# Optimization experiments

Measured on AMD Instinct MI355X. Metric: run time of the kernel, lower is better.

The kernel has to match this reference:

```python
import jax, jax.numpy as jnp
import numpy as np

THRESHOLD = 0.3
NEG_BIG = -2.0 ** 32  # matches tf -2**32 causal mask constant


def setup_inputs() -> dict:
    key = jax.random.key(0)
    kq, kt, kv = jax.random.split(key, 3)
    B, S, D = 16, 2048, 128
    Q = jax.random.normal(kq, (B, S, D), dtype=jnp.float32)
    T = jax.random.normal(kt, (B, S, D), dtype=jnp.float32)
    V = jax.random.normal(kv, (B, S, D), dtype=jnp.float32)
    return {"Q": Q, "T": T, "V": V}


def reference(Q, T, V):
    # scores: [B, S, S]
    A = jnp.einsum('bqd,bkd->bqk', Q, T)
    # Faithful to tf.where(A>thr, A, -2**32 * cast(A>thr)):
    # the false branch evaluates to 0 (mask is 0 there), NOT -2**32.
    A = jnp.where(A > THRESHOLD, A, jnp.zeros((), A.dtype))
    S = Q.shape[1]
    causal = jnp.triu(jnp.ones((S, S), dtype=bool), k=1)  # strictly upper = masked
    A = A + jnp.where(causal, jnp.asarray(NEG_BIG, A.dtype), jnp.zeros((), A.dtype))
    d_k = jnp.asarray(Q.shape[-1], A.dtype)
    A = A / jnp.sqrt(d_k)
    y = jax.nn.softmax(A, axis=-1)
    return jnp.einsum('bqk,bkd->bqd', y, V)
```

## Files before the change

### kernel.cpp

```cpp
#include <hip/hip_runtime.h>
#include <hip/hip_bf16.h>


#define S_LEN 2048
#define D_DIM 128
#define BQ 64
#define BK 64
#define THRESH 0.3f
#define SCALE 0.08838834764831845f

typedef __bf16 bf16x8 __attribute__((ext_vector_type(8)));
typedef float f32x4 __attribute__((ext_vector_type(4)));

__global__ void vt_kernel(const float* __restrict__ V, __bf16* __restrict__ Vt) {
    __shared__ float tile[64][65];
    int bid = blockIdx.x;
    int b  = bid >> 6;
    int t2 = bid & 63;
    int s0 = (t2 >> 1) * 64;
    int d0 = (t2 & 1) * 64;
    int tid = threadIdx.x;
    #pragma unroll
    for (int it = 0; it < 2; ++it) {
        int row = it * 32 + (tid >> 3);
        int c   = (tid & 7) * 8;
        const float* p = V + ((size_t)b * S_LEN + s0 + row) * D_DIM + d0 + c;
        *(f32x4*)(&tile[row][c])     = *(const f32x4*)p;
        *(f32x4*)(&tile[row][c + 4]) = *(const f32x4*)(p + 4);
    }
    __syncthreads();
    #pragma unroll
    for (int it = 0; it < 2; ++it) {
        int dr = it * 32 + (tid >> 3);
        int c  = (tid & 7) * 8;
        bf16x8 w;
        #pragma unroll
        for (int j = 0; j < 8; ++j) w[j] = (__bf16)tile[c + j][dr];
        *(bf16x8*)(Vt + ((size_t)b * D_DIM + d0 + dr) * S_LEN + s0 + c) = w;
    }
}

__global__ __launch_bounds__(256, 2)
void fa_kernel(const float* __restrict__ Q, const float* __restrict__ T,
               const __bf16* __restrict__ Vt, float* __restrict__ O) {
    __shared__ __bf16 Tt[64 * 136];
    __shared__ __bf16 Vl[128 * 72];
    __shared__ __bf16 Pl[4][16 * 72];

    int bid  = blockIdx.x;
    int b    = bid & 15;
    int half = bid >> 8;
    int idx  = (bid >> 4) & 15;
    int qt   = half == 0 ? (31 - idx) : idx;
    int q0   = qt * BQ;

    int tid  = threadIdx.x;
    int lane = tid & 63;
    int wave = tid >> 6;
    int col  = lane & 15;
    int quad = lane >> 4;

    const float* qptr = Q + ((size_t)b * S_LEN + (q0 + wave * 16 + col)) * D_DIM + quad * 8;
    bf16x8 qf[4];
    #pragma unroll
    for (int kk = 0; kk < 4; ++kk) {
        f32x4 a = *(const f32x4*)(qptr + kk * 32);
        f32x4 c = *(const f32x4*)(qptr + kk * 32 + 4);
        #pragma unroll
        for (int j = 0; j < 4; ++j) { qf[kk][j] = (__bf16)a[j]; qf[kk][4 + j] = (__bf16)c[j]; }
    }

    f32x4 oacc[8];
    #pragma unroll
    for (int dt = 0; dt < 8; ++dt) oacc[dt] = {0.f, 0.f, 0.f, 0.f};
    float lsum[4] = {0.f, 0.f, 0.f, 0.f};

    f32x4 tr[8]; bf16x8 vr[4];
    auto loadTiles = [&](int k0) {
        #pragma unroll
        for (int it = 0; it < 4; ++it) {
            int flat = it * 2048 + tid * 8;
            int row = flat >> 7, c = flat & 127;
            const float* p = T + ((size_t)b * S_LEN + k0 + row) * D_DIM + c;
            tr[2 * it]     = *(const f32x4*)p;
            tr[2 * it + 1] = *(const f32x4*)(p + 4);
        }
        #pragma unroll
        for (int it = 0; it < 4; ++it) {
            int flat = it * 2048 + tid * 8;
            int d = flat >> 6, kk2 = flat & 63;
            vr[it] = *(const bf16x8*)(Vt + ((size_t)b * D_DIM + d) * S_LEN + k0 + kk2);
        }
    };
    auto storeTiles = [&]() {
        #pragma unroll
        for (int it = 0; it < 4; ++it) {
            int flat = it * 2048 + tid * 8;
            int row = flat >> 7, c = flat & 127;
            bf16x8 w;
            #pragma unroll
            for (int j = 0; j < 4; ++j) {
                w[j]     = (__bf16)tr[2 * it][j];
                w[4 + j] = (__bf16)tr[2 * it + 1][j];
            }
            *(bf16x8*)(&Tt[row * 136 + c]) = w;
        }
        #pragma unroll
        for (int it = 0; it < 4; ++it) {
            int flat = it * 2048 + tid * 8;
            int d = flat >> 6, kk2 = flat & 63;
            *(bf16x8*)(&Vl[d * 72 + kk2]) = vr[it];
        }
    };

    loadTiles(0);
    storeTiles();
    __syncthreads();

    for (int kt = 0; kt <= qt; ++kt) {
        if (kt < qt) loadTiles((kt + 1) * BK);

        f32x4 sacc[4];
        #pragma unroll
        for (int t = 0; t < 4; ++t) {
            sacc[t] = {0.f, 0.f, 0.f, 0.f};
            #pragma unroll
            for (int kk = 0; kk < 4; ++kk) {
                bf16x8 bf = *(const bf16x8*)(&Tt[(t * 16 + col) * 136 + kk * 32 + quad * 8]);
                sacc[t] = __builtin_amdgcn_mfma_f32_16x16x32_bf16(qf[kk], bf, sacc[t], 0, 0, 0);
            }
        }

        bool diag = (kt == qt);
        float p[4][4];
        #pragma unroll
        for (int t = 0; t < 4; ++t)
            #pragma unroll
            for (int r = 0; r < 4; ++r) {
                float s = sacc[t][r];
                float e = __expf(s * SCALE);
                float w = (s > THRESH) ? e : 1.0f;
                if (diag && (t * 16 + col > wave * 16 + quad * 4 + r)) w = 0.0f;
                p[t][r] = w;
            }
        #pragma unroll
        for (int r = 0; r < 4; ++r)
            lsum[r] += (p[0][r] + p[1][r]) + (p[2][r] + p[3][r]);

        __bf16* pw = &Pl[wave][0];
        #pragma unroll
        for (int t = 0; t < 4; ++t)
            #pragma unroll
            for (int r = 0; r < 4; ++r)
                pw[(quad * 4 + r) * 72 + t * 16 + col] = (__bf16)p[t][r];

        asm volatile("s_waitcnt lgkmcnt(0)" ::: "memory");

        #pragma unroll
        for (int ks = 0; ks < 2; ++ks) {
            bf16x8 af = *(const bf16x8*)(&pw[col * 72 + ks * 32 + quad * 8]);
            #pragma unroll
            for (int dt = 0; dt < 8; ++dt) {
                bf16x8 bf = *(const bf16x8*)(&Vl[(dt * 16 + col) * 72 + ks * 32 + quad * 8]);
                oacc[dt] = __builtin_amdgcn_mfma_f32_16x16x32_bf16(af, bf, oacc[dt], 0, 0, 0);
            }
        }

        __syncthreads();
        if (kt < qt) storeTiles();
        __syncthreads();
    }

    #pragma unroll
    for (int r = 0; r < 4; ++r) {
        float l = lsum[r];
        l += __shfl_xor(l, 1);
        l += __shfl_xor(l, 2);
        l += __shfl_xor(l, 4);
        l += __shfl_xor(l, 8);
        lsum[r] = 1.0f / l;
    }
    float* optr = O + ((size_t)b * S_LEN + q0 + wave * 16) * D_DIM;
    #pragma unroll
    for (int dt = 0; dt < 8; ++dt)
        #pragma unroll
        for (int r = 0; r < 4; ++r)
            optr[(quad * 4 + r) * D_DIM + dt * 16 + col] = oacc[dt][r] * lsum[r];
}

extern "C" void kernel_launch(void* const* d_in, const int* in_sizes, int n_in,
                              void* d_out, int out_size, void* d_ws, size_t ws_size,
                              hipStream_t stream) {
    const float* Q = (const float*)d_in[0];
    const float* T = (const float*)d_in[1];
    const float* V = (const float*)d_in[2];
    __bf16* Vt = (__bf16*)d_ws;
    float* O   = (float*)d_out;

    vt_kernel<<<16 * 64, 256, 0, stream>>>(V, Vt);
    fa_kernel<<<16 * 32, 256, 0, stream>>>(Q, T, Vt, O);
}
```

Baseline: 136.1 us.

## Pair causal query tiles per block with split-K across two wave groups

Each 512-thread block now handles a pair of query tiles (pi and 31-pi) using two 256-thread groups. Group 0 computes the first 17 key tiles of the heavy tile. Group 1 finishes the light tile, then computes the remaining key tiles of the heavy tile, and the two partial results are merged through shared memory. The aim is a uniform 17-step workload per block, removing causal imbalance and tail effects. LDS padding is also replaced with XOR swizzling, which cuts bank conflicts but uses 80KB of LDS per block and halves the grid to 256 blocks, lowering occupancy.

```diff
diff --git a/kernel.cpp b/kernel.cpp
--- a/kernel.cpp
+++ b/kernel.cpp
@@ -40,46 +40,56 @@
     }
 }
 
-__global__ __launch_bounds__(256, 2)
+__global__ __launch_bounds__(512, 2)
 void fa_kernel(const float* __restrict__ Q, const float* __restrict__ T,
                const __bf16* __restrict__ Vt, float* __restrict__ O) {
-    __shared__ __bf16 Tt[64 * 136];
-    __shared__ __bf16 Vl[128 * 72];
-    __shared__ __bf16 Pl[4][16 * 72];
-
-    int bid  = blockIdx.x;
-    int b    = bid & 15;
-    int half = bid >> 8;
-    int idx  = (bid >> 4) & 15;
-    int qt   = half == 0 ? (31 - idx) : idx;
-    int q0   = qt * BQ;
-
-    int tid  = threadIdx.x;
-    int lane = tid & 63;
-    int wave = tid >> 6;
-    int col  = lane & 15;
-    int quad = lane >> 4;
-
-    const float* qptr = Q + ((size_t)b * S_LEN + (q0 + wave * 16 + col)) * D_DIM + quad * 8;
+    __shared__ __align__(16) unsigned char smem[81920];
+
+    const int bid = blockIdx.x;
+    const int b   = bid & 15;
+    const int pi  = bid >> 4;
+    const int qtH = 31 - pi;
+    const int L   = pi + 1;
+
+    const int tid   = threadIdx.x;
+    const int g     = tid >> 8;
+    const int tid_g = tid & 255;
+    const int lane  = tid & 63;
+    const int wg    = tid >> 6;
+    const int wv    = wg & 3;
+    const int col   = lane & 15;
+    const int quad  = lane >> 4;
+
+    unsigned char* Tt = smem + g * 16384;
+    unsigned char* Vl = smem + 32768 + g * 16384;
+    unsigned char* Pw = smem + 65536 + wg * 2048;
+
     bf16x8 qf[4];
-    #pragma unroll
-    for (int kk = 0; kk < 4; ++kk) {
-        f32x4 a = *(const f32x4*)(qptr + kk * 32);
-        f32x4 c = *(const f32x4*)(qptr + kk * 32 + 4);
-        #pragma unroll
-        for (int j = 0; j < 4; ++j) { qf[kk][j] = (__bf16)a[j]; qf[kk][4 + j] = (__bf16)c[j]; }
-    }
+    auto loadQ = [&](int qt) {
+        const float* qptr = Q + ((size_t)b * S_LEN + qt * BQ + wv * 16 + col) * D_DIM + quad * 8;
+        #pragma unroll
+        for (int kk = 0; kk < 4; ++kk) {
+            f32x4 a = *(const f32x4*)(qptr + kk * 32);
+            f32x4 c = *(const f32x4*)(qptr + kk * 32 + 4);
+            #pragma unroll
+            for (int j = 0; j < 4; ++j) { qf[kk][j] = (__bf16)a[j]; qf[kk][4 + j] = (__bf16)c[j]; }
+        }
+    };
 
     f32x4 oacc[8];
-    #pragma unroll
-    for (int dt = 0; dt < 8; ++dt) oacc[dt] = {0.f, 0.f, 0.f, 0.f};
-    float lsum[4] = {0.f, 0.f, 0.f, 0.f};
+    float lsum[4];
+    auto resetAcc = [&]() {
+        #pragma unroll
+        for (int dt = 0; dt < 8; ++dt) oacc[dt] = {0.f, 0.f, 0.f, 0.f};
+        #pragma unroll
+        for (int r = 0; r < 4; ++r) lsum[r] = 0.f;
+    };
 
     f32x4 tr[8]; bf16x8 vr[4];
     auto loadTiles = [&](int k0) {
         #pragma unroll
         for (int it = 0; it < 4; ++it) {
-            int flat = it * 2048 + tid * 8;
+            int flat = it * 2048 + tid_g * 8;
             int row = flat >> 7, c = flat & 127;
             const float* p = T + ((size_t)b * S_LEN + k0 + row) * D_DIM + c;
             tr[2 * it]     = *(const f32x4*)p;
@@ -87,7 +97,7 @@
         }
         #pragma unroll
         for (int it = 0; it < 4; ++it) {
-            int flat = it * 2048 + tid * 8;
+            int flat = it * 2048 + tid_g * 8;
             int d = flat >> 6, kk2 = flat & 63;
             vr[it] = *(const bf16x8*)(Vt + ((size_t)b * D_DIM + d) * S_LEN + k0 + kk2);
         }
@@ -95,7 +105,7 @@
     auto storeTiles = [&]() {
         #pragma unroll
         for (int it = 0; it < 4; ++it) {
-            int flat = it * 2048 + tid * 8;
+            int flat = it * 2048 + tid_g * 8;
             int row = flat >> 7, c = flat & 127;
             bf16x8 w;
             #pragma unroll
@@ -103,89 +113,152 @@
                 w[j]     = (__bf16)tr[2 * it][j];
                 w[4 + j] = (__bf16)tr[2 * it + 1][j];
             }
-            *(bf16x8*)(&Tt[row * 136 + c]) = w;
-        }
-        #pragma unroll
-        for (int it = 0; it < 4; ++it) {
-            int flat = it * 2048 + tid * 8;
+            *(bf16x8*)(Tt + row * 256 + ((c * 2) ^ ((row & 7) << 4))) = w;
+        }
+        #pragma unroll
+        for (int it = 0; it < 4; ++it) {
+            int flat = it * 2048 + tid_g * 8;
             int d = flat >> 6, kk2 = flat & 63;
-            *(bf16x8*)(&Vl[d * 72 + kk2]) = vr[it];
-        }
-    };
+            *(bf16x8*)(Vl + d * 128 + ((kk2 * 2) ^ ((d & 7) << 4))) = vr[it];
+        }
+    };
+
+    auto computeTile = [&](bool diag) {
+        f32x4 sacc[4];
+        #pragma unroll
+        for (int t = 0; t < 4; ++t) {
+            sacc[t] = {0.f, 0.f, 0.f, 0.f};
+            #pragma unroll
+            for (int kk = 0; kk < 4; ++kk) {
+                int row = t * 16 + col;
+                bf16x8 bf = *(const bf16x8*)(Tt + row * 256 + ((kk * 64 + quad * 16) ^ ((row & 7) << 4)));
+                sacc[t] = __builtin_amdgcn_mfma_f32_16x16x32_bf16(qf[kk], bf, sacc[t], 0, 0, 0);
+            }
+        }
+        float p[4][4];
+        #pragma unroll
+        for (int t = 0; t < 4; ++t)
+            #pragma unroll
+            for (int r = 0; r < 4; ++r) {
+                float s = sacc[t][r];
+                float e = __expf(s * SCALE);
+                float w = (s > THRESH) ? e : 1.0f;
+                if (diag && (t * 16 + col > wv * 16 + quad * 4 + r)) w = 0.0f;
+                p[t][r] = w;
+            }
+        #pragma unroll
+        for (int r = 0; r < 4; ++r)
+            lsum[r] += (p[0][r] + p[1][r]) + (p[2][r] + p[3][r]);
+
+        #pragma unroll
+        for (int t = 0; t < 4; ++t)
+            #pragma unroll
+            for (int r = 0; r < 4; ++r) {
+                int row = quad * 4 + r;
+                *(__bf16*)(Pw + row * 128 + (((t * 16 + col) * 2) ^ ((row & 7) << 4))) = (__bf16)p[t][r];
+            }
+        asm volatile("s_waitcnt lgkmcnt(0)" ::: "memory");
+
+        #pragma unroll
+        for (int ks = 0; ks < 2; ++ks) {
+            bf16x8 af = *(const bf16x8*)(Pw + col * 128 + ((ks * 64 + quad * 16) ^ ((col & 7) << 4)));
+            #pragma unroll
+            for (int dt = 0; dt < 8; ++dt) {
+                int row = dt * 16 + col;
+                bf16x8 bf = *(const bf16x8*)(Vl + row * 128 + ((ks * 64 + quad * 16) ^ ((row & 7) << 4)));
+                oacc[dt] = __builtin_amdgcn_mfma_f32_16x16x32_bf16(af, bf, oacc[dt], 0, 0, 0);
+            }
+        }
+    };
+
+    auto slotKT = [&](int s) -> int {
+        if (s >= 17) return -1;
+        if (g == 0) return s;
+        if (s < L)  return s;
+        if (s == L) return -1;
+        return s + 15 - pi;
+    };
+
+    resetAcc();
+    int qtile = (g == 0) ? qtH : pi;
+    loadQ(qtile);
 
     loadTiles(0);
     storeTiles();
     __syncthreads();
 
-    for (int kt = 0; kt <= qt; ++kt) {
-        if (kt < qt) loadTiles((kt + 1) * BK);
-
-        f32x4 sacc[4];
-        #pragma unroll
-        for (int t = 0; t < 4; ++t) {
-            sacc[t] = {0.f, 0.f, 0.f, 0.f};
-            #pragma unroll
-            for (int kk = 0; kk < 4; ++kk) {
-                bf16x8 bf = *(const bf16x8*)(&Tt[(t * 16 + col) * 136 + kk * 32 + quad * 8]);
-                sacc[t] = __builtin_amdgcn_mfma_f32_16x16x32_bf16(qf[kk], bf, sacc[t], 0, 0, 0);
-            }
-        }
-
-        bool diag = (kt == qt);
-        float p[4][4];
-        #pragma unroll
-        for (int t = 0; t < 4; ++t)
-            #pragma unroll
-            for (int r = 0; r < 4; ++r) {
-                float s = sacc[t][r];
-                float e = __expf(s * SCALE);
-                float w = (s > THRESH) ? e : 1.0f;
-                if (diag && (t * 16 + col > wave * 16 + quad * 4 + r)) w = 0.0f;
-                p[t][r] = w;
-            }
-        #pragma unroll
-        for (int r = 0; r < 4; ++r)
-            lsum[r] += (p[0][r] + p[1][r]) + (p[2][r] + p[3][r]);
-
-        __bf16* pw = &Pl[wave][0];
-        #pragma unroll
-        for (int t = 0; t < 4; ++t)
-            #pragma unroll
-            for (int r = 0; r < 4; ++r)
-                pw[(quad * 4 + r) * 72 + t * 16 + col] = (__bf16)p[t][r];
-
-        asm volatile("s_waitcnt lgkmcnt(0)" ::: "memory");
-
-        #pragma unroll
-        for (int ks = 0; ks < 2; ++ks) {
-            bf16x8 af = *(const bf16x8*)(&pw[col * 72 + ks * 32 + quad * 8]);
-            #pragma unroll
-            for (int dt = 0; dt < 8; ++dt) {
-                bf16x8 bf = *(const bf16x8*)(&Vl[(dt * 16 + col) * 72 + ks * 32 + quad * 8]);
-                oacc[dt] = __builtin_amdgcn_mfma_f32_16x16x32_bf16(af, bf, oacc[dt], 0, 0, 0);
-            }
-        }
-
+    for (int s = 0; s < 17; ++s) {
+        int kt  = slotKT(s);
+        int ktn = slotKT(s + 1);
+        if (ktn >= 0) loadTiles(ktn * BK);
+        if (kt >= 0) {
+            computeTile(kt == qtile);
+        } else {
+            float inv[4];
+            #pragma unroll
+            for (int r = 0; r < 4; ++r) {
+                float l = lsum[r];
+                l += __shfl_xor(l, 1); l += __shfl_xor(l, 2);
+                l += __shfl_xor(l, 4); l += __shfl_xor(l, 8);
+                inv[r] = 1.0f / l;
+            }
+            float* optr = O + ((size_t)b * S_LEN + (size_t)pi * BQ + wv * 16) * D_DIM;
+            #pragma unroll
+            for (int dt = 0; dt < 8; ++dt)
+                #pragma unroll
+                for (int r = 0; r < 4; ++r)
+                    optr[(quad * 4 + r) * D_DIM + dt * 16 + col] = oacc[dt][r] * inv[r];
+            resetAcc();
+            qtile = qtH;
+            loadQ(qtH);
+        }
         __syncthreads();
-        if (kt < qt) storeTiles();
+        if (ktn >= 0) storeTiles();
         __syncthreads();
     }
 
+    float lred[4];
     #pragma unroll
     for (int r = 0; r < 4; ++r) {
         float l = lsum[r];
-        l += __shfl_xor(l, 1);
-        l += __shfl_xor(l, 2);
-        l += __shfl_xor(l, 4);
-        l += __shfl_xor(l, 8);
-        lsum[r] = 1.0f / l;
-    }
-    float* optr = O + ((size_t)b * S_LEN + q0 + wave * 16) * D_DIM;
-    #pragma unroll
-    for (int dt = 0; dt < 8; ++dt)
-        #pragma unroll
-        for (int r = 0; r < 4; ++r)
-            optr[(quad * 4 + r) * D_DIM + dt * 16 + col] = oacc[dt][r] * lsum[r];
+        l += __shfl_xor(l, 1); l += __shfl_xor(l, 2);
+        l += __shfl_xor(l, 4); l += __shfl_xor(l, 8);
+        lred[r] = l;
+    }
+
+    if (g == 1) {
+        #pragma unroll
+        for (int dt = 0; dt < 8; ++dt)
+            #pragma unroll
+            for (int r = 0; r < 4; ++r) {
+                int row = wv * 16 + quad * 4 + r;
+                *(float*)(smem + row * 512 + (((dt * 16 + col) * 4) ^ ((row & 7) << 4))) = oacc[dt][r];
+            }
+        if (col == 0) {
+            #pragma unroll
+            for (int r = 0; r < 4; ++r)
+                *(float*)(smem + 65536 + (wv * 16 + quad * 4 + r) * 4) = lred[r];
+        }
+    }
+    __syncthreads();
+    if (g == 0) {
+        float inv[4];
+        #pragma unroll
+        for (int r = 0; r < 4; ++r) {
+            int row = wv * 16 + quad * 4 + r;
+            float lp = *(const float*)(smem + 65536 + row * 4);
+            inv[r] = 1.0f / (lred[r] + lp);
+        }
+        float* optr = O + ((size_t)b * S_LEN + (size_t)qtH * BQ + wv * 16) * D_DIM;
+        #pragma unroll
+        for (int dt = 0; dt < 8; ++dt)
+            #pragma unroll
+            for (int r = 0; r < 4; ++r) {
+                int row = wv * 16 + quad * 4 + r;
+                float part = *(const float*)(smem + row * 512 + (((dt * 16 + col) * 4) ^ ((row & 7) << 4)));
+                optr[(quad * 4 + r) * D_DIM + dt * 16 + col] = (oacc[dt][r] + part) * inv[r];
+            }
+    }
 }
 
 extern "C" void kernel_launch(void* const* d_in, const int* in_sizes, int n_in,
@@ -198,5 +271,5 @@
     float* O   = (float*)d_out;
 
     vt_kernel<<<16 * 64, 256, 0, stream>>>(V, Vt);
-    fa_kernel<<<16 * 32, 256, 0, stream>>>(Q, T, Vt, O);
+    fa_kernel<<<16 * 16, 512, 0, stream>>>(Q, T, Vt, O);
 }
```

New measurement: 135.3 us. About the same (-0.5%).
